# Optimization experiments

Hardware: AMD Instinct MI355X
Metric: run time of the kernel (lower is better)

Reference implementation:

```python
import jax, jax.numpy as jnp
import numpy as np

STDV = 1.0 / np.sqrt(512.0)


def _scan_lstm(x, Wih, Whh, bih, bhh):
    # x: [T, B, D]; gate order matches torch chunk: i, f, g, o
    T, B, _ = x.shape
    H = Whh.shape[0]
    # precompute input contribution for all timesteps at once (one big GEMM)
    xg = jnp.einsum('tbd,dg->tbg', x, Wih) + bih + bhh  # [T, B, 4H]

    def step(carry, xg_t):
        h, c = carry
        gates = xg_t + h @ Whh  # [B, 4H]
        i_g, f_g, g_g, o_g = jnp.split(gates, 4, axis=1)
        c = jax.nn.sigmoid(f_g) * c + jax.nn.sigmoid(i_g) * jnp.tanh(g_g)
        h = jax.nn.sigmoid(o_g) * jnp.tanh(c)
        return (h, c), (h, c)

    init = (jnp.zeros((B, H), x.dtype), jnp.zeros((B, H), x.dtype))
    _, (hs, cs) = jax.lax.scan(step, init, xg)
    return hs, cs  # each [T, B, H]


def setup_inputs() -> dict:
    key = jax.random.key(0)
    ks = jax.random.split(key, 9)
    T, B, D, H = 512, 64, 512, 512
    u = lambda k, shape: jax.random.uniform(k, shape, jnp.float32, -STDV, STDV)
    return {
        'x': jax.random.normal(ks[0], (T, B, D), jnp.float32),
        'Wih_f': u(ks[1], (D, 4 * H)),
        'Whh_f': u(ks[2], (H, 4 * H)),
        'bih_f': u(ks[3], (4 * H,)),
        'bhh_f': u(ks[4], (4 * H,)),
        'Wih_b': u(ks[5], (D, 4 * H)),
        'Whh_b': u(ks[6], (H, 4 * H)),
        'bih_b': u(ks[7], (4 * H,)),
        'bhh_b': u(ks[8], (4 * H,)),
    }


def reference(x, Wih_f, Whh_f, bih_f, bhh_f, Wih_b, Whh_b, bih_b, bhh_b):
    # num_layers=1, batch_first=False, init_states=None (zeros), as in source.
    # NOTE: the source's 'backward' net also iterates t in forward order
    # (a bug in the original), so both scans run in the same direction.
    hs_f, cs_f = _scan_lstm(x, Wih_f, Whh_f, bih_f, bhh_f)
    hs_b, cs_b = _scan_lstm(x, Wih_b, Whh_b, bih_b, bhh_b)
    h = jnp.concatenate([hs_f, hs_b], axis=-1)  # [T, B, 2H] == self.h[:, -1]
    c = jnp.concatenate([cs_f, cs_b], axis=-1)
    h_n = h[-1][None]  # [1, B, 2H] == self.h[-1] (num_layers=1)
    c_n = c[-1][None]
    return h, h_n, c_n
```

## Files before the change

### kernel.cpp

```cpp
#include <hip/hip_runtime.h>
#include <hip/hip_bf16.h>


typedef short s8v __attribute__((ext_vector_type(8)));
typedef float f4v __attribute__((ext_vector_type(4)));
typedef unsigned long long u2v __attribute__((ext_vector_type(2)));

#define T_STEPS 512
#define BATCH   64
#define KDIM    1024
#define NB_DIR  64
#define HS      8
#define COLS    32
#define NBLK    (2*NB_DIR)
#define WP      1032

#define WS_XB   0u
#define WS_WT   33554432u
#define WS_BIAS 41943040u
#define WS_HBUF 41959424u
#define WS_FLG  42221568u

__device__ __forceinline__ ushort f2bf(float f) {
  unsigned u = __builtin_bit_cast(unsigned, f);
  unsigned r = u + 0x7FFFu + ((u >> 16) & 1u);
  return (ushort)(r >> 16);
}

__global__ __launch_bounds__(256) void k_xcvt(const float* __restrict__ x,
                                              ushort* __restrict__ xb, int n8) {
  int i = blockIdx.x * 256 + threadIdx.x;
  if (i >= n8) return;
  size_t off = (size_t)i * 8;
  float4 a = *reinterpret_cast<const float4*>(x + off);
  float4 b = *reinterpret_cast<const float4*>(x + off + 4);
  s8v o;
  o[0] = (short)f2bf(a.x); o[1] = (short)f2bf(a.y);
  o[2] = (short)f2bf(a.z); o[3] = (short)f2bf(a.w);
  o[4] = (short)f2bf(b.x); o[5] = (short)f2bf(b.y);
  o[6] = (short)f2bf(b.z); o[7] = (short)f2bf(b.w);
  *reinterpret_cast<s8v*>(xb + off) = o;
}

__global__ __launch_bounds__(256) void k_wtprep(const float* __restrict__ WihF,
                                                const float* __restrict__ WhhF,
                                                const float* __restrict__ WihB,
                                                const float* __restrict__ WhhB,
                                                ushort* __restrict__ Wt) {
  int g = blockIdx.x * 256 + threadIdx.x;
  int d = g >> 11, col = g & 2047;
  const float* Wih = d ? WihB : WihF;
  const float* Whh = d ? WhhB : WhhF;
  int gate = col >> 9, j = col & 511;
  int nb = j >> 3, u = j & 7, p = (gate << 3) | u;
  ushort* dst = Wt + (((size_t)(d * NB_DIR + nb) * COLS + p) << 10);
  for (int k0 = 0; k0 < KDIM; k0 += 8) {
    s8v o;
#pragma unroll
    for (int i = 0; i < 8; ++i) {
      int k = k0 + i;
      float v = (k < 512) ? Wih[k * 2048 + col] : Whh[(k - 512) * 2048 + col];
      o[i] = (short)f2bf(v);
    }
    *reinterpret_cast<s8v*>(dst + k0) = o;
  }
}

__global__ __launch_bounds__(256) void k_init(const float* __restrict__ bihF,
                                              const float* __restrict__ bhhF,
                                              const float* __restrict__ bihB,
                                              const float* __restrict__ bhhB,
                                              float* __restrict__ bias,
                                              unsigned* __restrict__ hbuf_u32,
                                              unsigned* __restrict__ flg) {
  int g = blockIdx.x * 256 + threadIdx.x;
  if (g < 65536) hbuf_u32[g] = 0u;
  if (g < 2048) {
    bias[g]        = bihF[g] + bhhF[g];
    bias[2048 + g] = bihB[g] + bhhB[g];
  }
  if (g < 128) flg[g] = 0u;
}

__global__ __launch_bounds__(256, 1) void k_lstm(const ushort* __restrict__ xb,
                                                 const ushort* __restrict__ Wt,
                                                 const float* __restrict__ bias,
                                                 ushort* hbuf,
                                                 float* __restrict__ out,
                                                 unsigned* flags) {
  __shared__ ushort Wlds[COLS][WP];
  __shared__ float gates[BATCH][COLS + 1];
  __shared__ float cst[BATCH][HS];
  __shared__ float hlds[BATCH][HS];
  __shared__ float biasl[COLS];

  const int tid  = threadIdx.x;
  const int dir  = blockIdx.x & 1;
  const int nb   = blockIdx.x >> 1;
  const int lane = tid & 63;
  const int w    = tid >> 6;
  const int j0   = nb * HS;
  const int pc   = lane & 15;
  const int kgrp = (lane >> 4) << 3;

  const ushort* wsrc = Wt + ((size_t)(dir * NB_DIR + nb) << 15);
  for (int v = tid; v < COLS * 128; v += 256) {
    int p = v >> 7, kk = (v & 127) << 3;
    *reinterpret_cast<s8v*>(&Wlds[p][kk]) =
        *reinterpret_cast<const s8v*>(wsrc + (p << 10) + kk);
  }
  if (tid < COLS)
    biasl[tid] = bias[dir * 2048 + ((tid >> 3) << 9) + j0 + (tid & 7)];
  for (int v = tid; v < BATCH * HS; v += 256) cst[v >> 3][v & 7] = 0.f;
  __syncthreads();

  const int arow = (w << 4) + (lane & 15);

  float* outH  = out;
  float* outHn = out + (size_t)33554432;
  float* outCn = outHn + 65536;
  unsigned* myflag   = flags + (dir << 6) + nb;
  unsigned* dirflags = flags + (dir << 6);

  f4v acc0 = {0.f, 0.f, 0.f, 0.f}, acc1 = {0.f, 0.f, 0.f, 0.f};
  {
    const ushort* xa = xb + ((size_t)arow << 9) + kgrp;
#pragma unroll
    for (int kb = 0; kb < 16; ++kb) {
      s8v a  = *reinterpret_cast<const s8v*>(xa + (kb << 5));
      s8v wb0 = *reinterpret_cast<const s8v*>(&Wlds[pc][(kb << 5) + kgrp]);
      s8v wb1 = *reinterpret_cast<const s8v*>(&Wlds[16 + pc][(kb << 5) + kgrp]);
      acc0 = __builtin_amdgcn_mfma_f32_16x16x32_bf16(a, wb0, acc0, 0, 0, 0);
      acc1 = __builtin_amdgcn_mfma_f32_16x16x32_bf16(a, wb1, acc1, 0, 0, 0);
    }
  }

  for (int t = 0; t < T_STEPS; ++t) {
    if (t > 0) {
      if (tid < 64) {
        unsigned tgt = (unsigned)t;
        while (__hip_atomic_load(&dirflags[tid], __ATOMIC_RELAXED,
                                 __HIP_MEMORY_SCOPE_AGENT) < tgt)
          __builtin_amdgcn_s_sleep(1);
      }
      __syncthreads();
    }
    const ushort* ha = hbuf +
        ((size_t)(((dir << 1) | ((t + 1) & 1)) * BATCH + arow) << 9) + kgrp;
#pragma unroll
    for (int kb = 0; kb < 16; ++kb) {
      const unsigned long long* hq =
          reinterpret_cast<const unsigned long long*>(ha + (kb << 5));
      u2v q;
      q[0] = __hip_atomic_load(hq,     __ATOMIC_RELAXED, __HIP_MEMORY_SCOPE_AGENT);
      q[1] = __hip_atomic_load(hq + 1, __ATOMIC_RELAXED, __HIP_MEMORY_SCOPE_AGENT);
      s8v a = __builtin_bit_cast(s8v, q);
      s8v wb0 = *reinterpret_cast<const s8v*>(&Wlds[pc][512 + (kb << 5) + kgrp]);
      s8v wb1 = *reinterpret_cast<const s8v*>(&Wlds[16 + pc][512 + (kb << 5) + kgrp]);
      acc0 = __builtin_amdgcn_mfma_f32_16x16x32_bf16(a, wb0, acc0, 0, 0, 0);
      acc1 = __builtin_amdgcn_mfma_f32_16x16x32_bf16(a, wb1, acc1, 0, 0, 0);
    }
    {
      int r0 = (w << 4) + ((lane >> 4) << 2);
#pragma unroll
      for (int r = 0; r < 4; ++r) {
        gates[r0 + r][pc]      = acc0[r];
        gates[r0 + r][16 + pc] = acc1[r];
      }
    }
    __syncthreads();
    {
      int b = tid >> 2, up = (tid & 3) << 1;
      float h2[2], c2[2];
#pragma unroll
      for (int e = 0; e < 2; ++e) {
        int u = up + e;
        float ig = gates[b][u]      + biasl[u];
        float fg = gates[b][8 + u]  + biasl[8 + u];
        float gg = gates[b][16 + u] + biasl[16 + u];
        float og = gates[b][24 + u] + biasl[24 + u];
        float cp = cst[b][u];
        float si = 1.f / (1.f + __expf(-ig));
        float sf = 1.f / (1.f + __expf(-fg));
        float so = 1.f / (1.f + __expf(-og));
        float tg = 1.f - 2.f / (__expf(2.f * gg) + 1.f);
        float c  = sf * cp + si * tg;
        float tc = 1.f - 2.f / (__expf(2.f * c) + 1.f);
        float h  = so * tc;
        cst[b][u] = c;
        hlds[b][u] = h;
        h2[e] = h; c2[e] = c;
      }
      unsigned pk = (unsigned)f2bf(h2[0]) | ((unsigned)f2bf(h2[1]) << 16);
      unsigned* hb = (unsigned*)(hbuf +
          ((size_t)(((dir << 1) | (t & 1)) * BATCH + b) << 9) + j0 + up);
      __hip_atomic_store(hb, pk, __ATOMIC_RELAXED, __HIP_MEMORY_SCOPE_AGENT);
      if (t == T_STEPS - 1) {
        size_t oc = ((size_t)b << 10) + (dir << 9) + j0 + up;
        __builtin_nontemporal_store(h2[0], outHn + oc);
        __builtin_nontemporal_store(h2[1], outHn + oc + 1);
        __builtin_nontemporal_store(c2[0], outCn + oc);
        __builtin_nontemporal_store(c2[1], outCn + oc + 1);
      }
    }
    __syncthreads();
    if (tid == 0)
      __hip_atomic_store(myflag, (unsigned)(t + 1), __ATOMIC_RELAXED,
                         __HIP_MEMORY_SCOPE_AGENT);
    if (tid < 64) {
      const f4v* hp = reinterpret_cast<const f4v*>(&hlds[tid][0]);
      f4v v0 = hp[0], v1 = hp[1];
      float* dst = outH + ((size_t)t << 16) + ((size_t)tid << 10) + (dir << 9) + j0;
      __builtin_nontemporal_store(v0, reinterpret_cast<f4v*>(dst));
      __builtin_nontemporal_store(v1, reinterpret_cast<f4v*>(dst + 4));
    }
    acc0 = (f4v){0.f, 0.f, 0.f, 0.f};
    acc1 = (f4v){0.f, 0.f, 0.f, 0.f};
    if (t < T_STEPS - 1) {
      const ushort* xa = xb + (((size_t)(t + 1) * BATCH + arow) << 9) + kgrp;
#pragma unroll
      for (int kb = 0; kb < 16; ++kb) {
        s8v a  = *reinterpret_cast<const s8v*>(xa + (kb << 5));
        s8v wb0 = *reinterpret_cast<const s8v*>(&Wlds[pc][(kb << 5) + kgrp]);
        s8v wb1 = *reinterpret_cast<const s8v*>(&Wlds[16 + pc][(kb << 5) + kgrp]);
        acc0 = __builtin_amdgcn_mfma_f32_16x16x32_bf16(a, wb0, acc0, 0, 0, 0);
        acc1 = __builtin_amdgcn_mfma_f32_16x16x32_bf16(a, wb1, acc1, 0, 0, 0);
      }
    }
  }
}

extern "C" void kernel_launch(void* const* d_in, const int* in_sizes, int n_in,
                              void* d_out, int out_size, void* d_ws, size_t ws_size,
                              hipStream_t stream) {
  const float* x    = (const float*)d_in[0];
  const float* WihF = (const float*)d_in[1];
  const float* WhhF = (const float*)d_in[2];
  const float* bihF = (const float*)d_in[3];
  const float* bhhF = (const float*)d_in[4];
  const float* WihB = (const float*)d_in[5];
  const float* WhhB = (const float*)d_in[6];
  const float* bihB = (const float*)d_in[7];
  const float* bhhB = (const float*)d_in[8];

  char* ws = (char*)d_ws;
  ushort*   xb   = (ushort*)(ws + WS_XB);
  ushort*   Wt   = (ushort*)(ws + WS_WT);
  float*    bias = (float*)(ws + WS_BIAS);
  ushort*   hbuf = (ushort*)(ws + WS_HBUF);
  unsigned* flg  = (unsigned*)(ws + WS_FLG);

  k_xcvt<<<8192, 256, 0, stream>>>(x, xb, 2097152);
  k_wtprep<<<16, 256, 0, stream>>>(WihF, WhhF, WihB, WhhB, Wt);
  k_init<<<256, 256, 0, stream>>>(bihF, bhhF, bihB, bhhB, bias,
                                  (unsigned*)hbuf, flg);
  k_lstm<<<NBLK, 256, 0, stream>>>(xb, Wt, bias, hbuf, (float*)d_out, flg);
}
```

Before: 4.164 ms.

## Exchange hidden state through fp32 output tensor instead of separate bf16 buffer

```diff
diff --git a/kernel.cpp b/kernel.cpp
--- a/kernel.cpp
+++ b/kernel.cpp
@@ -4,7 +4,6 @@
 
 typedef short s8v __attribute__((ext_vector_type(8)));
 typedef float f4v __attribute__((ext_vector_type(4)));
-typedef unsigned long long u2v __attribute__((ext_vector_type(2)));
 
 #define T_STEPS 512
 #define BATCH   64
@@ -18,8 +17,7 @@
 #define WS_XB   0u
 #define WS_WT   33554432u
 #define WS_BIAS 41943040u
-#define WS_HBUF 41959424u
-#define WS_FLG  42221568u
+#define WS_FLG  41959424u
 
 __device__ __forceinline__ ushort f2bf(float f) {
   unsigned u = __builtin_bit_cast(unsigned, f);
@@ -71,10 +69,8 @@
                                               const float* __restrict__ bihB,
                                               const float* __restrict__ bhhB,
                                               float* __restrict__ bias,
-                                              unsigned* __restrict__ hbuf_u32,
                                               unsigned* __restrict__ flg) {
   int g = blockIdx.x * 256 + threadIdx.x;
-  if (g < 65536) hbuf_u32[g] = 0u;
   if (g < 2048) {
     bias[g]        = bihF[g] + bhhF[g];
     bias[2048 + g] = bihB[g] + bhhB[g];
@@ -85,13 +81,11 @@
 __global__ __launch_bounds__(256, 1) void k_lstm(const ushort* __restrict__ xb,
                                                  const ushort* __restrict__ Wt,
                                                  const float* __restrict__ bias,
-                                                 ushort* hbuf,
                                                  float* __restrict__ out,
                                                  unsigned* flags) {
   __shared__ ushort Wlds[COLS][WP];
   __shared__ float gates[BATCH][COLS + 1];
   __shared__ float cst[BATCH][HS];
-  __shared__ float hlds[BATCH][HS];
   __shared__ float biasl[COLS];
 
   const int tid  = threadIdx.x;
@@ -122,6 +116,8 @@
   unsigned* myflag   = flags + (dir << 6) + nb;
   unsigned* dirflags = flags + (dir << 6);
 
+  const float* hsrc = out + ((size_t)arow << 10) + (dir << 9) + kgrp;
+
   f4v acc0 = {0.f, 0.f, 0.f, 0.f}, acc1 = {0.f, 0.f, 0.f, 0.f};
   {
     const ushort* xa = xb + ((size_t)arow << 9) + kgrp;
@@ -144,21 +140,23 @@
           __builtin_amdgcn_s_sleep(1);
       }
       __syncthreads();
-    }
-    const ushort* ha = hbuf +
-        ((size_t)(((dir << 1) | ((t + 1) & 1)) * BATCH + arow) << 9) + kgrp;
-#pragma unroll
-    for (int kb = 0; kb < 16; ++kb) {
-      const unsigned long long* hq =
-          reinterpret_cast<const unsigned long long*>(ha + (kb << 5));
-      u2v q;
-      q[0] = __hip_atomic_load(hq,     __ATOMIC_RELAXED, __HIP_MEMORY_SCOPE_AGENT);
-      q[1] = __hip_atomic_load(hq + 1, __ATOMIC_RELAXED, __HIP_MEMORY_SCOPE_AGENT);
-      s8v a = __builtin_bit_cast(s8v, q);
-      s8v wb0 = *reinterpret_cast<const s8v*>(&Wlds[pc][512 + (kb << 5) + kgrp]);
-      s8v wb1 = *reinterpret_cast<const s8v*>(&Wlds[16 + pc][512 + (kb << 5) + kgrp]);
-      acc0 = __builtin_amdgcn_mfma_f32_16x16x32_bf16(a, wb0, acc0, 0, 0, 0);
-      acc1 = __builtin_amdgcn_mfma_f32_16x16x32_bf16(a, wb1, acc1, 0, 0, 0);
+      const float* ha = hsrc + (((size_t)t - 1) << 16);
+#pragma unroll
+      for (int kb = 0; kb < 16; ++kb) {
+        const f4v* hp = reinterpret_cast<const f4v*>(ha + (kb << 5));
+        f4v lo = hp[0], hi = hp[1];
+        unsigned q0, q1, q2, q3;
+        asm("v_cvt_pk_bf16_f32 %0, %1, %2" : "=v"(q0) : "v"(lo[0]), "v"(lo[1]));
+        asm("v_cvt_pk_bf16_f32 %0, %1, %2" : "=v"(q1) : "v"(lo[2]), "v"(lo[3]));
+        asm("v_cvt_pk_bf16_f32 %0, %1, %2" : "=v"(q2) : "v"(hi[0]), "v"(hi[1]));
+        asm("v_cvt_pk_bf16_f32 %0, %1, %2" : "=v"(q3) : "v"(hi[2]), "v"(hi[3]));
+        unsigned uv[4] = {q0, q1, q2, q3};
+        s8v a = __builtin_bit_cast(s8v, uv);
+        s8v wb0 = *reinterpret_cast<const s8v*>(&Wlds[pc][512 + (kb << 5) + kgrp]);
+        s8v wb1 = *reinterpret_cast<const s8v*>(&Wlds[16 + pc][512 + (kb << 5) + kgrp]);
+        acc0 = __builtin_amdgcn_mfma_f32_16x16x32_bf16(a, wb0, acc0, 0, 0, 0);
+        acc1 = __builtin_amdgcn_mfma_f32_16x16x32_bf16(a, wb1, acc1, 0, 0, 0);
+      }
     }
     {
       int r0 = (w << 4) + ((lane >> 4) << 2);
@@ -188,15 +186,15 @@
         float tc = 1.f - 2.f / (__expf(2.f * c) + 1.f);
         float h  = so * tc;
         cst[b][u] = c;
-        hlds[b][u] = h;
         h2[e] = h; c2[e] = c;
       }
-      unsigned pk = (unsigned)f2bf(h2[0]) | ((unsigned)f2bf(h2[1]) << 16);
-      unsigned* hb = (unsigned*)(hbuf +
-          ((size_t)(((dir << 1) | (t & 1)) * BATCH + b) << 9) + j0 + up);
-      __hip_atomic_store(hb, pk, __ATOMIC_RELAXED, __HIP_MEMORY_SCOPE_AGENT);
+      union { float f[2]; unsigned long long q; } hu;
+      hu.f[0] = h2[0]; hu.f[1] = h2[1];
+      size_t oc = ((size_t)b << 10) + (dir << 9) + j0 + up;
+      unsigned long long* hb =
+          reinterpret_cast<unsigned long long*>(outH + ((size_t)t << 16) + oc);
+      __hip_atomic_store(hb, hu.q, __ATOMIC_RELAXED, __HIP_MEMORY_SCOPE_AGENT);
       if (t == T_STEPS - 1) {
-        size_t oc = ((size_t)b << 10) + (dir << 9) + j0 + up;
         __builtin_nontemporal_store(h2[0], outHn + oc);
         __builtin_nontemporal_store(h2[1], outHn + oc + 1);
         __builtin_nontemporal_store(c2[0], outCn + oc);
@@ -207,13 +205,6 @@
     if (tid == 0)
       __hip_atomic_store(myflag, (unsigned)(t + 1), __ATOMIC_RELAXED,
                          __HIP_MEMORY_SCOPE_AGENT);
-    if (tid < 64) {
-      const f4v* hp = reinterpret_cast<const f4v*>(&hlds[tid][0]);
-      f4v v0 = hp[0], v1 = hp[1];
-      float* dst = outH + ((size_t)t << 16) + ((size_t)tid << 10) + (dir << 9) + j0;
-      __builtin_nontemporal_store(v0, reinterpret_cast<f4v*>(dst));
-      __builtin_nontemporal_store(v1, reinterpret_cast<f4v*>(dst + 4));
-    }
     acc0 = (f4v){0.f, 0.f, 0.f, 0.f};
     acc1 = (f4v){0.f, 0.f, 0.f, 0.f};
     if (t < T_STEPS - 1) {
@@ -247,12 +238,10 @@
   ushort*   xb   = (ushort*)(ws + WS_XB);
   ushort*   Wt   = (ushort*)(ws + WS_WT);
   float*    bias = (float*)(ws + WS_BIAS);
-  ushort*   hbuf = (ushort*)(ws + WS_HBUF);
   unsigned* flg  = (unsigned*)(ws + WS_FLG);
 
   k_xcvt<<<8192, 256, 0, stream>>>(x, xb, 2097152);
   k_wtprep<<<16, 256, 0, stream>>>(WihF, WhhF, WihB, WhhB, Wt);
-  k_init<<<256, 256, 0, stream>>>(bihF, bhhF, bihB, bhhB, bias,
-                                  (unsigned*)hbuf, flg);
-  k_lstm<<<NBLK, 256, 0, stream>>>(xb, Wt, bias, hbuf, (float*)d_out, flg);
-}
+  k_init<<<8, 256, 0, stream>>>(bihF, bhhF, bihB, bhhB, bias, flg);
+  k_lstm<<<NBLK, 256, 0, stream>>>(xb, Wt, bias, (float*)d_out, flg);
+}
```

Result: no change. 4.183 ms (+0.5%).
